# Optimization experiments

Hardware: AMD Instinct MI355X
Metric: run time of the kernel (lower is better)

The kernel has to match this reference:

```python
import jax, jax.numpy as jnp
import numpy as np

B, L, H, DI, N, R, K = 1, 1024, 2048, 4096, 16, 128, 4


def setup_inputs() -> dict:
    key = jax.random.key(0)
    ks = jax.random.split(key, 12)
    s = 0.02
    x = jax.random.normal(ks[0], (B, L, H), jnp.float32)
    W_in_states = jax.random.normal(ks[1], (DI, H), jnp.float32) * s
    W_in_gates = jax.random.normal(ks[2], (DI, H), jnp.float32) * s
    conv_w = jax.random.normal(ks[3], (DI, K), jnp.float32) * 0.2
    conv_b = jax.random.normal(ks[4], (DI,), jnp.float32) * 0.02
    W_dt = jax.random.normal(ks[5], (R, DI), jnp.float32) * s
    W_b = jax.random.normal(ks[6], (N, DI), jnp.float32) * s
    W_c = jax.random.normal(ks[7], (N, DI), jnp.float32) * s
    W_dtproj = jax.random.normal(ks[8], (DI, R), jnp.float32) * 0.1
    # dt bias so softplus(dt) is in a realistic small range
    b_dtproj = jax.random.uniform(ks[9], (DI,), jnp.float32, minval=-5.0, maxval=-3.0)
    A_log = jnp.log(jnp.broadcast_to(jnp.arange(1, N + 1, dtype=jnp.float32), (DI, N)))
    D = jnp.ones((DI,), jnp.float32)
    W_out = jax.random.normal(ks[10], (H, DI), jnp.float32) * s
    return {"x": x, "W_in_states": W_in_states, "W_in_gates": W_in_gates,
            "conv_w": conv_w, "conv_b": conv_b, "W_dt": W_dt, "W_b": W_b,
            "W_c": W_c, "W_dtproj": W_dtproj, "b_dtproj": b_dtproj,
            "A_log": A_log, "D": D, "W_out": W_out}


def _silu(v):
    return v * jax.nn.sigmoid(v)


def reference(x, W_in_states, W_in_gates, conv_w, conv_b, W_dt, W_b, W_c,
              W_dtproj, b_dtproj, A_log, D, W_out):
    b, l, _ = x.shape
    # input projections -> [B, DI, L]
    hs = jnp.einsum('blh,dh->bdl', x, W_in_states)
    gate = jnp.einsum('blh,dh->bdl', x, W_in_gates)
    # causal depthwise conv1d (kernel K, left pad K-1, truncate to L)
    k = conv_w.shape[-1]
    xpad = jnp.pad(hs, ((0, 0), (0, 0), (k - 1, 0)))
    conv = sum(conv_w[None, :, j, None] * xpad[:, :, j:j + l] for j in range(k))
    conv = conv + conv_b[None, :, None]
    hs = _silu(conv)                       # [B, DI, L]
    hst = hs.transpose(0, 2, 1)            # [B, L, DI]
    # data-dependent SSM params
    time_step = jnp.einsum('bld,rd->blr', hst, W_dt)           # [B, L, R]
    dt = jax.nn.softplus(time_step @ W_dtproj.T + b_dtproj)    # [B, L, DI]
    Bm = jnp.einsum('bld,nd->bln', hst, W_b)                   # [B, L, N]
    Cm = jnp.einsum('bld,nd->bln', hst, W_c)                   # [B, L, N]
    A = -jnp.exp(A_log)                                        # [DI, N]
    dt_bdl = dt.transpose(0, 2, 1)                             # [B, DI, L]
    dA = jnp.exp(A[None, :, None, :] * dt_bdl[:, :, :, None])  # [B, DI, L, N]
    dBu = dt_bdl[:, :, :, None] * Bm[:, None, :, :] * hs[:, :, :, None]
    # sequential selective scan over L
    dA_l = dA.transpose(2, 0, 1, 3)    # [L, B, DI, N]
    dBu_l = dBu.transpose(2, 0, 1, 3)

    def step(s, inp):
        a, bu = inp
        s = a * s + bu
        return s, s

    init = jnp.zeros((b, hs.shape[1], A_log.shape[1]), hs.dtype)
    _, h = jax.lax.scan(step, init, (dA_l, dBu_l))   # [L, B, DI, N]
    y = jnp.einsum('lbdn,bln->bdl', h, Cm)           # contract state dim
    y = y + hs * D[None, :, None]
    y = y * _silu(gate)
    out = jnp.einsum('bdl,od->blo', y, W_out)        # [B, L, H]
    return out
```

## Files before the change

### kernel.cpp

```cpp
#include <hip/hip_runtime.h>

#define SEQ 1024
#define HID 2048
#define DIN 4096
#define NST 16
#define RNK 128
#define CHN 64
#define CLEN 16

typedef __attribute__((ext_vector_type(4))) float f32x4;
typedef __attribute__((ext_vector_type(4))) __bf16 bf16x4v;
typedef __attribute__((ext_vector_type(8))) __bf16 bf16x8v;
typedef __attribute__((ext_vector_type(8))) unsigned short u16x8;

#define GPTR(p) ((const __attribute__((address_space(1))) void*)(p))
#define LPTR(p) ((__attribute__((address_space(3))) void*)(p))

__device__ __forceinline__ unsigned short f2bf(float v) {
  unsigned u = __builtin_bit_cast(unsigned, v);
  u = (u + 0x7fffu + ((u >> 16) & 1u)) >> 16;
  return (unsigned short)u;
}
__device__ __forceinline__ float softplus_f(float x) {
  return (x > 20.f) ? x : log1pf(__expf(x));
}
__device__ __forceinline__ float silu_f(float x) {
  return x / (1.f + __expf(-x));
}

#define CV_NX  (SEQ*HID)
#define CV_NW  (DIN*HID)
#define CV_NDT (RNK*DIN)
#define CV_NB  (NST*DIN)
#define CV_NPD (32*DIN)
#define CV_NWO (HID*DIN)
#define CV_TOT (CV_NX + 2*CV_NW + CV_NDT + 2*CV_NB + CV_NPD + CV_NDT + CV_NWO)

__global__ __launch_bounds__(256) void cvt_all(
    const float* __restrict__ x, const float* __restrict__ wis,
    const float* __restrict__ wig, const float* __restrict__ wdt,
    const float* __restrict__ wb, const float* __restrict__ wc,
    const float* __restrict__ wdtp, const float* __restrict__ wout,
    unsigned short* __restrict__ x_bf, unsigned short* __restrict__ wis_bf,
    unsigned short* __restrict__ wig_bf, unsigned short* __restrict__ wcat_bf,
    unsigned short* __restrict__ wdtp_bf, unsigned short* __restrict__ wout_bf)
{
  size_t j = ((size_t)blockIdx.x * 256 + threadIdx.x) * 8;
  const float* src = nullptr; unsigned short* dst;
  if (j < CV_NX) { src = x + j; dst = x_bf + j; }
  else if ((j -= CV_NX) < CV_NW) { src = wis + j; dst = wis_bf + j; }
  else if ((j -= CV_NW) < CV_NW) { src = wig + j; dst = wig_bf + j; }
  else if ((j -= CV_NW) < CV_NDT) { src = wdt + j; dst = wcat_bf + j; }
  else if ((j -= CV_NDT) < CV_NB) { src = wb + j; dst = wcat_bf + (size_t)128*DIN + j; }
  else if ((j -= CV_NB) < CV_NB) { src = wc + j; dst = wcat_bf + (size_t)144*DIN + j; }
  else if ((j -= CV_NB) < CV_NPD) { dst = wcat_bf + (size_t)160*DIN + j; }
  else if ((j -= CV_NPD) < CV_NDT) { src = wdtp + j; dst = wdtp_bf + j; }
  else { j -= CV_NDT; src = wout + j; dst = wout_bf + j; }
  u16x8 o = {};
  if (src) {
    f32x4 a = *(const f32x4*)src;
    f32x4 b = *(const f32x4*)(src + 4);
#pragma unroll
    for (int i = 0; i < 4; i++) { o[i] = f2bf(a[i]); o[4 + i] = f2bf(b[i]); }
  }
  *(u16x8*)dst = o;
}

template<int EPI>
__global__ __launch_bounds__(256) void gemm128(
    const unsigned short* __restrict__ Ag, const unsigned short* __restrict__ Bg,
    float* __restrict__ Cg, const float* __restrict__ bias,
    int Msz, int Nsz, int Kstride, int Kiter)
{
  __shared__ __align__(16) unsigned short As[128 * 32];
  __shared__ __align__(16) unsigned short Bs[128 * 32];
  const int kz = blockIdx.z;
  Ag += (size_t)kz * Kiter;
  Bg += (size_t)kz * Kiter;
  Cg += (size_t)kz * Msz * Nsz;
  const int tid = threadIdx.x;
  const int m0 = blockIdx.x * 128, n0 = blockIdx.y * 128;
  const int lane = tid & 63, w = tid >> 6;
  const int wm = w >> 1, wn = w & 1;
  const int lg = lane >> 4, lr = lane & 15;
  const int srow = w * 32 + (lane >> 2);
  const int sch = (lane & 3) * 8;
  const unsigned short* Ag0 = Ag + (size_t)(m0 + srow) * Kstride + sch;
  const unsigned short* Bg0 = Bg + (size_t)(n0 + srow) * Kstride + sch;
  unsigned short* AsW = As + w * 1024;
  unsigned short* BsW = Bs + w * 1024;
  f32x4 acc[4][4] = {};
  for (int k0 = 0; k0 < Kiter; k0 += 32) {
    __builtin_amdgcn_global_load_lds(GPTR(Ag0 + k0), LPTR(AsW), 16, 0, 0);
    __builtin_amdgcn_global_load_lds(GPTR(Ag0 + 16 * Kstride + k0), LPTR(AsW + 512), 16, 0, 0);
    __builtin_amdgcn_global_load_lds(GPTR(Bg0 + k0), LPTR(BsW), 16, 0, 0);
    __builtin_amdgcn_global_load_lds(GPTR(Bg0 + 16 * Kstride + k0), LPTR(BsW + 512), 16, 0, 0);
    __syncthreads();
    bf16x8v af[4], bfv[4];
#pragma unroll
    for (int mi = 0; mi < 4; mi++)
      af[mi] = *(const bf16x8v*)&As[(wm * 64 + mi * 16 + lr) * 32 + lg * 8];
#pragma unroll
    for (int ni = 0; ni < 4; ni++)
      bfv[ni] = *(const bf16x8v*)&Bs[(wn * 64 + ni * 16 + lr) * 32 + lg * 8];
#pragma unroll
    for (int mi = 0; mi < 4; mi++)
#pragma unroll
      for (int ni = 0; ni < 4; ni++)
        acc[mi][ni] = __builtin_amdgcn_mfma_f32_16x16x32_bf16(af[mi], bfv[ni], acc[mi][ni], 0, 0, 0);
    __syncthreads();
  }
#pragma unroll
  for (int mi = 0; mi < 4; mi++) {
#pragma unroll
    for (int ni = 0; ni < 4; ni++) {
      const int col = n0 + wn * 64 + ni * 16 + lr;
#pragma unroll
      for (int r = 0; r < 4; r++) {
        const int row = m0 + wm * 64 + mi * 16 + lg * 4 + r;
        float v = acc[mi][ni][r];
        if (EPI == 1) v = softplus_f(v + bias[col]);
        Cg[(size_t)row * Nsz + col] = v;
      }
    }
  }
}

template<int EPI>
__global__ __launch_bounds__(256) void gemm_nt(
    const unsigned short* __restrict__ Ag, const unsigned short* __restrict__ Bg,
    float* __restrict__ Cg, const float* __restrict__ bias,
    int Msz, int Nsz, int Kstride, int Kiter)
{
  __shared__ __align__(16) unsigned short As[128][40];
  __shared__ __align__(16) unsigned short Bs[64][40];
  const int kz = blockIdx.z;
  Ag += (size_t)kz * Kiter;
  Bg += (size_t)kz * Kiter;
  Cg += (size_t)kz * Msz * Nsz;
  const int tid = threadIdx.x;
  const int m0 = blockIdx.x * 128, n0 = blockIdx.y * 64;
  const int lane = tid & 63, w = tid >> 6;
  const int wm = w >> 1, wn = w & 1;
  const int lg = lane >> 4, lr = lane & 15;
  const int r4 = tid >> 2, c8 = (tid & 3) * 8;
  f32x4 acc[4][2] = {};
  for (int k0 = 0; k0 < Kiter; k0 += 32) {
    uint4 a0 = *(const uint4*)(Ag + (size_t)(m0 + r4) * Kstride + k0 + c8);
    uint4 a1 = *(const uint4*)(Ag + (size_t)(m0 + 64 + r4) * Kstride + k0 + c8);
    uint4 b0 = *(const uint4*)(Bg + (size_t)(n0 + r4) * Kstride + k0 + c8);
    *(uint4*)&As[r4][c8] = a0;
    *(uint4*)&As[64 + r4][c8] = a1;
    *(uint4*)&Bs[r4][c8] = b0;
    __syncthreads();
    bf16x8v af[4], bfr[2];
#pragma unroll
    for (int mi = 0; mi < 4; mi++) {
      const int row = wm * 64 + mi * 16 + lr;
      bf16x4v lo = *(const bf16x4v*)&As[row][4 * lg];
      bf16x4v hi = *(const bf16x4v*)&As[row][16 + 4 * lg];
      af[mi] = __builtin_shufflevector(lo, hi, 0, 1, 2, 3, 4, 5, 6, 7);
    }
#pragma unroll
    for (int ni = 0; ni < 2; ni++) {
      const int row = wn * 32 + ni * 16 + lr;
      bf16x4v lo = *(const bf16x4v*)&Bs[row][4 * lg];
      bf16x4v hi = *(const bf16x4v*)&Bs[row][16 + 4 * lg];
      bfr[ni] = __builtin_shufflevector(lo, hi, 0, 1, 2, 3, 4, 5, 6, 7);
    }
#pragma unroll
    for (int mi = 0; mi < 4; mi++)
#pragma unroll
      for (int ni = 0; ni < 2; ni++)
        acc[mi][ni] = __builtin_amdgcn_mfma_f32_16x16x32_bf16(af[mi], bfr[ni], acc[mi][ni], 0, 0, 0);
    __syncthreads();
  }
#pragma unroll
  for (int mi = 0; mi < 4; mi++) {
#pragma unroll
    for (int ni = 0; ni < 2; ni++) {
      const int col = n0 + wn * 32 + ni * 16 + lr;
#pragma unroll
      for (int r = 0; r < 4; r++) {
        const int row = m0 + wm * 64 + mi * 16 + lg * 4 + r;
        float v = acc[mi][ni][r];
        if (EPI == 1) v = softplus_f(v + bias[col]);
        Cg[(size_t)row * Nsz + col] = v;
      }
    }
  }
}

__global__ __launch_bounds__(256) void conv_silu(
    const float* __restrict__ pg, const float* __restrict__ cw,
    const float* __restrict__ cb, float* __restrict__ hs,
    unsigned short* __restrict__ hs_bf)
{
  int idx = blockIdx.x * 256 + threadIdx.x;
  int l = idx >> 12, d = idx & (DIN - 1);
  float acc = cb[d];
#pragma unroll
  for (int j = 0; j < 4; j++) {
    int ll = l + j - 3;
    float v = (ll >= 0) ? pg[(size_t)ll * 8192 + d] : 0.f;
    acc = fmaf(cw[d * 4 + j], v, acc);
  }
  float r = silu_f(acc);
  hs[idx] = r;
  hs_bf[idx] = f2bf(r);
}

__global__ __launch_bounds__(256) void reduce_ts(
    const float* __restrict__ c2p, float* __restrict__ c2,
    unsigned short* __restrict__ ts_bf)
{
  int i = blockIdx.x * 256 + threadIdx.x;
  float s = 0.f;
#pragma unroll
  for (int z = 0; z < 8; z++) s += c2p[(size_t)z * SEQ * 192 + i];
  c2[i] = s;
  int l = i / 192, col = i - l * 192;
  if (col < 128) ts_bf[l * 128 + col] = f2bf(s);
}

__global__ __launch_bounds__(256) void reduce_out(
    const float* __restrict__ p, float* __restrict__ out)
{
  int i = (blockIdx.x * 256 + threadIdx.x) * 4;
  float4 a = *(const float4*)&p[i];
  float4 b = *(const float4*)&p[(size_t)SEQ * HID + i];
  a.x += b.x; a.y += b.y; a.z += b.z; a.w += b.w;
  *(float4*)&out[i] = a;
}

__global__ __launch_bounds__(256) void scan_phase1(
    const float* __restrict__ dt, const float* __restrict__ hs,
    const float* __restrict__ c2, const float* __restrict__ alog,
    float* __restrict__ Pbuf, float* __restrict__ Sbuf)
{
  __shared__ float B_ch[CLEN][16];
  const int tid = threadIdx.x;
  const int d = blockIdx.x * 256 + tid;
  const int c = blockIdx.y;
  const int l0 = c * CLEN;
  B_ch[tid >> 4][tid & 15] = c2[(size_t)(l0 + (tid >> 4)) * 192 + 128 + (tid & 15)];
  float a[16];
#pragma unroll
  for (int i = 0; i < 16; i++) a[i] = -__expf(alog[(size_t)d * 16 + i]);
  __syncthreads();
  float s[16] = {};
  float P[16];
#pragma unroll
  for (int i = 0; i < 16; i++) P[i] = 1.f;
  for (int t = 0; t < CLEN; t++) {
    float dtv = dt[(size_t)(l0 + t) * DIN + d];
    float u = hs[(size_t)(l0 + t) * DIN + d];
    float w = dtv * u;
#pragma unroll
    for (int n = 0; n < 16; n++) {
      float dA = __expf(a[n] * dtv);
      s[n] = fmaf(dA, s[n], w * B_ch[t][n]);
      P[n] *= dA;
    }
  }
  size_t base = ((size_t)c * DIN + d) * 16;
#pragma unroll
  for (int i = 0; i < 4; i++) {
    *(float4*)&Sbuf[base + 4 * i] = *(float4*)&s[4 * i];
    *(float4*)&Pbuf[base + 4 * i] = *(float4*)&P[4 * i];
  }
}

__global__ __launch_bounds__(256) void scan_phase2(
    const float* __restrict__ Pbuf, float* __restrict__ Sbuf)
{
  size_t idx = (size_t)blockIdx.x * 256 + threadIdx.x;
  const size_t stride = (size_t)DIN * 16;
  float s = 0.f;
#pragma unroll 4
  for (int c = 0; c < CHN; c++) {
    float Pv = Pbuf[c * stride + idx];
    float Sv = Sbuf[c * stride + idx];
    Sbuf[c * stride + idx] = s;
    s = fmaf(Pv, s, Sv);
  }
}

__global__ __launch_bounds__(256) void scan_phase3(
    const float* __restrict__ dt, const float* __restrict__ hs,
    const float* __restrict__ pg, const float* __restrict__ c2,
    const float* __restrict__ alog, const float* __restrict__ Dv,
    const float* __restrict__ sig, unsigned short* __restrict__ ygT)
{
  __shared__ float B_ch[CLEN][16], C_ch[CLEN][16];
  const int tid = threadIdx.x;
  const int d = blockIdx.x * 256 + tid;
  const int c = blockIdx.y;
  const int l0 = c * CLEN;
  {
    int t = tid >> 4, n = tid & 15;
    B_ch[t][n] = c2[(size_t)(l0 + t) * 192 + 128 + n];
    C_ch[t][n] = c2[(size_t)(l0 + t) * 192 + 144 + n];
  }
  float a[16];
#pragma unroll
  for (int i = 0; i < 16; i++) a[i] = -__expf(alog[(size_t)d * 16 + i]);
  const float Dd = Dv[d];
  float s[16];
  size_t base = ((size_t)c * DIN + d) * 16;
#pragma unroll
  for (int i = 0; i < 4; i++) *(float4*)&s[4 * i] = *(const float4*)&sig[base + 4 * i];
  __syncthreads();
  for (int t = 0; t < CLEN; t++) {
    float dtv = dt[(size_t)(l0 + t) * DIN + d];
    float u = hs[(size_t)(l0 + t) * DIN + d];
    float g = pg[(size_t)(l0 + t) * 8192 + 4096 + d];
    float w = dtv * u;
    float y = 0.f;
#pragma unroll
    for (int n = 0; n < 16; n++) {
      float dA = __expf(a[n] * dtv);
      s[n] = fmaf(dA, s[n], w * B_ch[t][n]);
      y = fmaf(s[n], C_ch[t][n], y);
    }
    float o = (y + u * Dd) * silu_f(g);
    ygT[(size_t)(l0 + t) * DIN + d] = f2bf(o);
  }
}

extern "C" void kernel_launch(void* const* d_in, const int* in_sizes, int n_in,
                              void* d_out, int out_size, void* d_ws, size_t ws_size,
                              hipStream_t stream) {
  const float* x     = (const float*)d_in[0];
  const float* wis   = (const float*)d_in[1];
  const float* wig   = (const float*)d_in[2];
  const float* convw = (const float*)d_in[3];
  const float* convb = (const float*)d_in[4];
  const float* wdt   = (const float*)d_in[5];
  const float* wb    = (const float*)d_in[6];
  const float* wc    = (const float*)d_in[7];
  const float* wdtp  = (const float*)d_in[8];
  const float* bdtp  = (const float*)d_in[9];
  const float* alog  = (const float*)d_in[10];
  const float* Dv    = (const float*)d_in[11];
  const float* wout  = (const float*)d_in[12];

  char* ws = (char*)d_ws;
  size_t off = 0;
  auto alloc = [&](size_t bytes) { void* p = ws + off; off += (bytes + 255) & ~(size_t)255; return p; };
  unsigned short* x_bf    = (unsigned short*)alloc((size_t)SEQ * HID * 2);
  unsigned short* wis_bf  = (unsigned short*)alloc((size_t)DIN * HID * 2);
  unsigned short* wig_bf  = (unsigned short*)alloc((size_t)DIN * HID * 2);
  unsigned short* wcat_bf = (unsigned short*)alloc((size_t)192 * DIN * 2);
  unsigned short* wdtp_bf = (unsigned short*)alloc((size_t)DIN * RNK * 2);
  unsigned short* wout_bf = (unsigned short*)alloc((size_t)HID * DIN * 2);
  float* pg    = (float*)alloc((size_t)SEQ * 8192 * 4);
  float* hs2   = (float*)alloc((size_t)SEQ * DIN * 4);
  unsigned short* hs_bf = (unsigned short*)alloc((size_t)SEQ * DIN * 2);
  float* c2    = (float*)alloc((size_t)SEQ * 192 * 4);
  float* c2p   = (float*)alloc((size_t)8 * SEQ * 192 * 4);
  unsigned short* ts_bf = (unsigned short*)alloc((size_t)SEQ * RNK * 2);
  float* dtbuf = (float*)alloc((size_t)SEQ * DIN * 4);
  unsigned short* ygT_bf = (unsigned short*)alloc((size_t)SEQ * DIN * 2);
  if (off > ws_size) return;
  float* Pbuf = (float*)wis_bf;
  float* Sbuf = (float*)wig_bf;
  float* op_part = dtbuf;

  cvt_all<<<CV_TOT / 2048, 256, 0, stream>>>(x, wis, wig, wdt, wb, wc, wdtp, wout,
                                             x_bf, wis_bf, wig_bf, wcat_bf, wdtp_bf, wout_bf);
  gemm128<0><<<dim3(SEQ / 128, 8192 / 128), 256, 0, stream>>>(x_bf, wis_bf, pg, nullptr, SEQ, 8192, HID, HID);
  conv_silu<<<(SEQ * DIN) / 256, 256, 0, stream>>>(pg, convw, convb, hs2, hs_bf);
  gemm_nt<0><<<dim3(SEQ / 128, 192 / 64, 8), 256, 0, stream>>>(hs_bf, wcat_bf, c2p, nullptr, SEQ, 192, DIN, DIN / 8);
  reduce_ts<<<(SEQ * 192) / 256, 256, 0, stream>>>(c2p, c2, ts_bf);
  gemm_nt<1><<<dim3(SEQ / 128, DIN / 64), 256, 0, stream>>>(ts_bf, wdtp_bf, dtbuf, bdtp, SEQ, DIN, RNK, RNK);
  scan_phase1<<<dim3(DIN / 256, CHN), 256, 0, stream>>>(dtbuf, hs2, c2, alog, Pbuf, Sbuf);
  scan_phase2<<<(DIN * NST) / 256, 256, 0, stream>>>(Pbuf, Sbuf);
  scan_phase3<<<dim3(DIN / 256, CHN), 256, 0, stream>>>(dtbuf, hs2, pg, c2, alog, Dv, Sbuf, ygT_bf);
  gemm128<0><<<dim3(SEQ / 128, HID / 128, 2), 256, 0, stream>>>(ygT_bf, wout_bf, op_part, nullptr, SEQ, HID, DIN, DIN / 2);
  reduce_out<<<(SEQ * HID) / 1024, 256, 0, stream>>>(op_part, (float*)d_out);
}
```

Before: 254.3 us.

## Triple-buffer LDS tiles in gemm128 and swizzle workgroup order

Replaces the single-buffer load/sync/compute loop in the bf16 MFMA GEMM with a three-stage LDS ring. Loads run two K-steps ahead, gated by vmcnt waits and one barrier per iteration, so global-to-LDS traffic can overlap MFMA work. It also remaps workgroup IDs in groups of 8 to improve L2 reuse. The cost is triple the LDS footprint, which may reduce occupancy. Correctness depends on vmcnt(4) matching exactly one in-flight stage, and the swizzle assumes the workgroup count is divisible by 8.

```diff
diff --git a/kernel.cpp b/kernel.cpp
--- a/kernel.cpp
+++ b/kernel.cpp
@@ -72,14 +72,18 @@
     float* __restrict__ Cg, const float* __restrict__ bias,
     int Msz, int Nsz, int Kstride, int Kiter)
 {
-  __shared__ __align__(16) unsigned short As[128 * 32];
-  __shared__ __align__(16) unsigned short Bs[128 * 32];
+  __shared__ __align__(16) unsigned short As[3][128 * 32];
+  __shared__ __align__(16) unsigned short Bs[3][128 * 32];
   const int kz = blockIdx.z;
   Ag += (size_t)kz * Kiter;
   Bg += (size_t)kz * Kiter;
   Cg += (size_t)kz * Msz * Nsz;
+  const int nwg = gridDim.x * gridDim.y;
+  const int orig = blockIdx.y * gridDim.x + blockIdx.x;
+  const int swz = (orig & 7) * (nwg >> 3) + (orig >> 3);
+  const int bx = swz % gridDim.x, by = swz / gridDim.x;
   const int tid = threadIdx.x;
-  const int m0 = blockIdx.x * 128, n0 = blockIdx.y * 128;
+  const int m0 = bx * 128, n0 = by * 128;
   const int lane = tid & 63, w = tid >> 6;
   const int wm = w >> 1, wn = w & 1;
   const int lg = lane >> 4, lr = lane & 15;
@@ -87,28 +91,43 @@
   const int sch = (lane & 3) * 8;
   const unsigned short* Ag0 = Ag + (size_t)(m0 + srow) * Kstride + sch;
   const unsigned short* Bg0 = Bg + (size_t)(n0 + srow) * Kstride + sch;
-  unsigned short* AsW = As + w * 1024;
-  unsigned short* BsW = Bs + w * 1024;
+  const int wo = w * 1024;
+
+  auto stage = [&](int b, int k0) {
+    __builtin_amdgcn_global_load_lds(GPTR(Ag0 + k0), LPTR(&As[b][wo]), 16, 0, 0);
+    __builtin_amdgcn_global_load_lds(GPTR(Ag0 + 16 * Kstride + k0), LPTR(&As[b][wo + 512]), 16, 0, 0);
+    __builtin_amdgcn_global_load_lds(GPTR(Bg0 + k0), LPTR(&Bs[b][wo]), 16, 0, 0);
+    __builtin_amdgcn_global_load_lds(GPTR(Bg0 + 16 * Kstride + k0), LPTR(&Bs[b][wo + 512]), 16, 0, 0);
+  };
+
+  const int nt = Kiter >> 5;
+  stage(0, 0);
+  stage(1, 32);
   f32x4 acc[4][4] = {};
-  for (int k0 = 0; k0 < Kiter; k0 += 32) {
-    __builtin_amdgcn_global_load_lds(GPTR(Ag0 + k0), LPTR(AsW), 16, 0, 0);
-    __builtin_amdgcn_global_load_lds(GPTR(Ag0 + 16 * Kstride + k0), LPTR(AsW + 512), 16, 0, 0);
-    __builtin_amdgcn_global_load_lds(GPTR(Bg0 + k0), LPTR(BsW), 16, 0, 0);
-    __builtin_amdgcn_global_load_lds(GPTR(Bg0 + 16 * Kstride + k0), LPTR(BsW + 512), 16, 0, 0);
-    __syncthreads();
+  int cur = 0, pf = 2;
+  for (int t = 0; t < nt; ++t) {
+    if (t < nt - 1) {
+      asm volatile("s_waitcnt vmcnt(4)" ::: "memory");
+    } else {
+      asm volatile("s_waitcnt vmcnt(0)" ::: "memory");
+    }
+    __builtin_amdgcn_s_barrier();
+    asm volatile("" ::: "memory");
+    if (t + 2 < nt) stage(pf, (t + 2) * 32);
     bf16x8v af[4], bfv[4];
 #pragma unroll
     for (int mi = 0; mi < 4; mi++)
-      af[mi] = *(const bf16x8v*)&As[(wm * 64 + mi * 16 + lr) * 32 + lg * 8];
+      af[mi] = *(const bf16x8v*)&As[cur][(wm * 64 + mi * 16 + lr) * 32 + lg * 8];
 #pragma unroll
     for (int ni = 0; ni < 4; ni++)
-      bfv[ni] = *(const bf16x8v*)&Bs[(wn * 64 + ni * 16 + lr) * 32 + lg * 8];
+      bfv[ni] = *(const bf16x8v*)&Bs[cur][(wn * 64 + ni * 16 + lr) * 32 + lg * 8];
 #pragma unroll
     for (int mi = 0; mi < 4; mi++)
 #pragma unroll
       for (int ni = 0; ni < 4; ni++)
         acc[mi][ni] = __builtin_amdgcn_mfma_f32_16x16x32_bf16(af[mi], bfv[ni], acc[mi][ni], 0, 0, 0);
-    __syncthreads();
+    cur = (cur == 2) ? 0 : cur + 1;
+    pf = (pf == 2) ? 0 : pf + 1;
   }
 #pragma unroll
   for (int mi = 0; mi < 4; mi++) {
```

Result: faster. 238.8 us (-6.1%).
